# Kernel optimization log

Hardware: AMD Instinct MI355X
Metric: run time of the kernel (lower is better)

Reference implementation:

```python
import jax, jax.numpy as jnp
import numpy as np

B, T, C = 1, 2048, 2048
H, G, D = 16, 4, 128   # n_head, n_query_groups, head_size
I = 8192               # intermediate_size


def _hv(x, alpha, beta):
    # ParamHeaveside forward: alpha * heaviside(x - beta)
    return (alpha * (x - beta > 0).astype(x.dtype)).astype(x.dtype)


def _normed_linear(x, w, scale):
    # NormedLinear: column-center then L2-normalize columns (dim=0), scaled
    w = w - w.mean(axis=0, keepdims=True)
    n = jnp.maximum(jnp.sqrt((w * w).sum(axis=0, keepdims=True)), 1e-12)
    return x @ (scale * w / n).T


def _rope(t, cos, sin):
    # non-interleaved rotary (rotate-half), cos/sin: [T, D/2]
    half = t.shape[-1] // 2
    t1, t2 = t[..., :half], t[..., half:]
    c, s = cos[None, :, None, :], sin[None, :, None, :]
    return jnp.concatenate([t1 * c - t2 * s, t1 * s + t2 * c], axis=-1)


def _block(x, cos, sin, attn_w, proj_w, proj_scale, fc_w, mlp_proj_w, mlp_proj_scale,
           in_alpha, in_beta, q_alpha, q_beta, k_alpha, k_beta,
           out_alpha, out_beta, act1_alpha, act1_beta, act2_alpha, act2_beta, hv):
    q_per_kv = H // G
    h = hv(x, in_alpha, in_beta)                      # encoder_input (norm is identity)
    qkv = (h @ attn_w.T).reshape(B, T, G, q_per_kv + 2, D)
    q = qkv[:, :, :, :q_per_kv, :].reshape(B, T, H, D)
    k = qkv[:, :, :, q_per_kv, :]                     # [B,T,G,D]
    v = qkv[:, :, :, q_per_kv + 1, :]                 # [B,T,G,D]
    q = hv(_rope(q, cos, sin), q_alpha, q_beta)
    k = hv(_rope(k, cos, sin), k_alpha, k_beta)
    q = q.transpose(0, 2, 1, 3)                       # [B,H,T,D]
    k = jnp.repeat(k.transpose(0, 2, 1, 3), q_per_kv, axis=1)
    v = jnp.repeat(v.transpose(0, 2, 1, 3), q_per_kv, axis=1)
    scores = jnp.einsum('bhtd,bhsd->bhts', q, k) * (1.0 / D)  # scale = 1/head_size
    causal = jnp.tril(jnp.ones((T, T), bool))
    w = jnp.where(causal[None, None], jax.nn.relu(scores), 0.0)  # relu-attention
    y = jnp.einsum('bhts,bhsd->bhtd', w, v).transpose(0, 2, 1, 3).reshape(B, T, C)
    y = _normed_linear(hv(y, out_alpha, out_beta), proj_w, proj_scale)
    x = x + y
    m = hv(x, act1_alpha, act1_beta) @ fc_w.T
    m = _normed_linear(hv(m, act2_alpha, act2_beta), mlp_proj_w, mlp_proj_scale)
    return x + m


def setup_inputs() -> dict:
    key = jax.random.key(0)
    ks = jax.random.split(key, 8)
    rn = lambda k, s, sc=0.02: (jax.random.normal(k, s) * sc).astype(jnp.float32)
    theta = 1.0 / (10000.0 ** (jnp.arange(0, D, 2, dtype=jnp.float32) / D))
    idx = jnp.outer(jnp.arange(T, dtype=jnp.float32), theta)
    return {
        'x': jax.random.normal(ks[0], (B, T, C), dtype=jnp.float32),
        'cos': jnp.cos(idx), 'sin': jnp.sin(idx),
        'attn_w': rn(ks[1], ((H + 2 * G) * D, C)),
        'proj_w': rn(ks[2], (C, C)), 'proj_scale': jnp.float32(0.01),
        'fc_w': rn(ks[3], (I, C)),
        'mlp_proj_w': rn(ks[4], (C, I)), 'mlp_proj_scale': jnp.float32(0.01),
        'in_alpha': jnp.full((C,), 0.5, jnp.float32), 'in_beta': rn(ks[5], (C,), 0.01),
        'q_alpha': jnp.full((D,), 0.5, jnp.float32), 'q_beta': jnp.zeros((D,), jnp.float32),
        'k_alpha': jnp.full((D,), 0.5, jnp.float32), 'k_beta': jnp.zeros((D,), jnp.float32),
        'out_alpha': jnp.full((C,), 0.5, jnp.float32), 'out_beta': rn(ks[6], (C,), 0.01),
        'act1_alpha': jnp.full((C,), 0.5, jnp.float32), 'act1_beta': rn(ks[7], (C,), 0.01),
        'act2_alpha': jnp.full((I,), 0.5, jnp.float32), 'act2_beta': jnp.zeros((I,), jnp.float32),
    }


def reference(x, cos, sin, attn_w, proj_w, proj_scale, fc_w, mlp_proj_w, mlp_proj_scale,
              in_alpha, in_beta, q_alpha, q_beta, k_alpha, k_beta,
              out_alpha, out_beta, act1_alpha, act1_beta, act2_alpha, act2_beta):
    return _block(x, cos, sin, attn_w, proj_w, proj_scale, fc_w, mlp_proj_w, mlp_proj_scale,
                  in_alpha, in_beta, q_alpha, q_beta, k_alpha, k_beta,
                  out_alpha, out_beta, act1_alpha, act1_beta, act2_alpha, act2_beta, _hv)
```

## Files before the change

### kernel.cpp

```cpp
#include <hip/hip_runtime.h>

typedef __attribute__((ext_vector_type(8))) short short8;
typedef __attribute__((ext_vector_type(4))) float f32x4;
typedef __attribute__((ext_vector_type(4))) int i32x4;

constexpr int TT = 2048, CC = 2048, HQ = 16, GG = 4, DD = 128, IC = 8192;

__device__ __forceinline__ ushort f2b(float f) {
  union { float f; unsigned u; } v; v.f = f;
  unsigned r = v.u + 0x7fffu + ((v.u >> 16) & 1u);
  return (ushort)(r >> 16);
}
__device__ __forceinline__ float b2f(ushort u) {
  union { unsigned u; float f; } v; v.u = ((unsigned)u) << 16; return v.f;
}
__device__ __forceinline__ char q8(float eff, float r) {
  float q = rintf(eff * r);
  q = fminf(fmaxf(q, -127.f), 127.f);
  return (char)(int)q;
}
__device__ __forceinline__ unsigned cvt_pk_bf16(float a, float b) {
  unsigned r;
  asm("v_cvt_pk_bf16_f32 %0, %1, %2" : "=v"(r) : "v"(a), "v"(b));
  return r;
}

__device__ __forceinline__ void gload16(const void* g, void* l) {
  __builtin_amdgcn_global_load_lds(
      (const __attribute__((address_space(1))) void*)g,
      (__attribute__((address_space(3))) void*)l, 16, 0, 0);
}

#define BAR()    __builtin_amdgcn_s_barrier()
#define PRIO1()  __builtin_amdgcn_s_setprio(1)
#define PRIO0()  __builtin_amdgcn_s_setprio(0)

template<int EPI>
__global__ __launch_bounds__(512, 2)
void gemm_i8(const char* __restrict__ A, const char* __restrict__ B,
             void* __restrict__ C0, const float* __restrict__ s,
             const float* __restrict__ beta, int M, int N, int K, int kc)
{
  __shared__ alignas(16) char lds[131072];
  const int tid = threadIdx.x;
  const int l = tid & 63, w = tid >> 6;
  const int fl = l & 15, fh = l >> 4;
  const int wrm = w >> 2, wcn = w & 3;
  const int m0 = blockIdx.y * 256, n0 = blockIdx.x * 256;
  const int kBeg = blockIdx.z * kc;
  const int kEnd = (kBeg + kc < K) ? kBeg + kc : K;
  const int nt = (kEnd - kBeg) >> 7;

  i32x4 acc[8][4] = {};

  const int srow = tid >> 3;
  const int scol = ((tid & 7) ^ (srow & 7)) * 16;
  const char* Ag = A + (size_t)(m0 + srow) * K + kBeg + scol;
  const char* Bg = B + (size_t)(n0 + srow) * K + kBeg + scol;

  auto stage_half = [&](int tile, int h) {
    const char* base = (h < 2) ? Ag : Bg;
    const int half = h & 1;
    const char* g = base + (size_t)(half * 128) * K + tile * 128;
    char* d = lds + (tile & 1) * 65536 + ((h < 2) ? 0 : 32768) + half * 16384 + tid * 16;
    gload16(g, d);
    gload16(g + (size_t)64 * K, d + 8192);
  };

  auto readA = [&](i32x4 (&dst)[4][2], int buf, int mofs) {
#pragma unroll
    for (int mf = 0; mf < 4; ++mf)
#pragma unroll
      for (int ks = 0; ks < 2; ++ks) {
        int row = wrm * 128 + (mofs + mf) * 16 + fl;
        dst[mf][ks] = *(const i32x4*)(lds + buf * 65536 + row * 128 +
                                      (((ks * 4 + fh) ^ (row & 7)) * 16));
      }
  };
  auto readB = [&](i32x4 (&dst)[2][2], int buf, int nofs) {
#pragma unroll
    for (int nf = 0; nf < 2; ++nf)
#pragma unroll
      for (int ks = 0; ks < 2; ++ks) {
        int row = wcn * 64 + (nofs + nf) * 16 + fl;
        dst[nf][ks] = *(const i32x4*)(lds + buf * 65536 + 32768 + row * 128 +
                                      (((ks * 4 + fh) ^ (row & 7)) * 16));
      }
  };
  auto mmQ = [&](i32x4 (&a)[4][2], i32x4 (&b)[2][2], int mo, int no) {
    PRIO1();
#pragma unroll
    for (int mf = 0; mf < 4; ++mf)
#pragma unroll
      for (int nf = 0; nf < 2; ++nf)
#pragma unroll
        for (int ks = 0; ks < 2; ++ks)
          acc[mo + mf][no + nf] = __builtin_amdgcn_mfma_i32_16x16x64_i8(
              a[mf][ks], b[nf][ks], acc[mo + mf][no + nf], 0, 0, 0);
    PRIO0();
  };

  stage_half(0, 0); stage_half(0, 1); stage_half(0, 2); stage_half(0, 3);
  if (nt > 1) {
    stage_half(1, 2); stage_half(1, 3);
    asm volatile("s_waitcnt vmcnt(4)" ::: "memory");
  } else {
    asm volatile("s_waitcnt vmcnt(0)" ::: "memory");
  }
  BAR();

  for (int t = 0; t < nt; ++t) {
    const int buf = t & 1;
    i32x4 A0[4][2], A1[4][2], B0[2][2], B1[2][2];

    readA(A0, buf, 0);
    readB(B0, buf, 0);
    if (t + 1 < nt) stage_half(t + 1, 0);
    BAR();
    mmQ(A0, B0, 0, 0);

    readB(B1, buf, 2);
    if (t + 1 < nt) stage_half(t + 1, 1);
    BAR();
    mmQ(A0, B1, 0, 2);

    readA(A1, buf, 4);
    BAR();
    mmQ(A1, B0, 4, 0);

    if (t + 2 < nt) { stage_half(t + 2, 2); stage_half(t + 2, 3); }
    if (t <= nt - 3) asm volatile("s_waitcnt vmcnt(4)" ::: "memory");
    else             asm volatile("s_waitcnt vmcnt(0)" ::: "memory");
    BAR();
    mmQ(A1, B1, 4, 2);
  }

  const int orow0 = m0 + wrm * 128 + fh * 4;
  const int ocol0 = n0 + wcn * 64 + fl;
#pragma unroll
  for (int mf = 0; mf < 8; ++mf) {
#pragma unroll
    for (int nf = 0; nf < 4; ++nf) {
      const int c = ocol0 + nf * 16;
      const float sc = s[c];
#pragma unroll
      for (int j = 0; j < 4; ++j) {
        const int r = orow0 + mf * 16 + j;
        const size_t o = (size_t)r * N + c;
        float v = (float)acc[mf][nf][j] * sc;
        if constexpr (EPI == 1) {
          ((char*)C0)[o] = (v - beta[c] > 0.f) ? (char)1 : (char)0;
        } else {
          ((ushort*)C0 + (size_t)blockIdx.z * M * N)[o] = f2b(v);
        }
      }
    }
  }
}

template<int NS, int MODE>
__global__ void reduce_kernel(const ushort* p0, const ushort* p1, const ushort* p2, const ushort* p3,
                              const float* resid, float* outf, char* outb,
                              const float* beta, int n4, int cols)
{
  const ushort* ps[4] = {p0, p1, p2, p3};
  for (int i = blockIdx.x * blockDim.x + threadIdx.x; i < n4; i += gridDim.x * blockDim.x) {
    float4 s = ((const float4*)resid)[i];
#pragma unroll
    for (int z = 0; z < NS; ++z) {
      ushort4 q = ((const ushort4*)ps[z])[i];
      s.x += b2f(q.x); s.y += b2f(q.y); s.z += b2f(q.z); s.w += b2f(q.w);
    }
    ((float4*)outf)[i] = s;
    if constexpr (MODE == 1) {
      int c = (i * 4) & (cols - 1);
      char4 r;
      r.x = (s.x - beta[c] > 0.f) ? 1 : 0;
      r.y = (s.y - beta[c + 1] > 0.f) ? 1 : 0;
      r.z = (s.z - beta[c + 2] > 0.f) ? 1 : 0;
      r.w = (s.w - beta[c + 3] > 0.f) ? 1 : 0;
      ((char4*)outb)[i] = r;
    }
  }
}

__global__ __launch_bounds__(256, 4)
void attn_kernel(const ushort* __restrict__ qb, const ushort* __restrict__ kb,
                 const ushort* __restrict__ vt, char* __restrict__ hy,
                 const float* __restrict__ obeta)
{
  __shared__ alignas(16) ushort Ks[64 * 128];
  __shared__ alignas(16) ushort Vs[128 * 64];
  __shared__ alignas(16) ushort Ps[64 * 64];
  const int bx = blockIdx.x;
  const int h = blockIdx.y;
  const int qi = (h & 8) ? bx : (31 - bx);
  const int g = h >> 2;
  const int q0 = qi * 64;
  const int tid = threadIdx.x;
  const int w = tid >> 6, l = tid & 63;
  const int fl = l & 15, fh = l >> 4;

  auto stageK = [&](int s0t) {
#pragma unroll
    for (int i = 0; i < 4; ++i) {
      int row = w * 16 + i * 4 + (l >> 4);
      int c16 = (l & 15) ^ (row & 7);
      gload16(kb + (size_t)g * TT * DD + (size_t)(s0t + row) * DD + c16 * 8,
              (char*)Ks + (w << 12) + (i << 10) + (l << 4));
    }
  };
  auto stageV = [&](int s0t) {
#pragma unroll
    for (int i = 0; i < 4; ++i) {
      int d = w * 32 + i * 8 + (l >> 3);
      int c16 = (l & 7) ^ (d & 7);
      gload16(vt + (size_t)g * DD * TT + (size_t)d * TT + s0t + c16 * 8,
              (char*)Vs + (w << 12) + (i << 10) + (l << 4));
    }
  };

  short8 qf[4];
  {
    const ushort* qp = qb + (size_t)h * TT * DD + (size_t)(q0 + w * 16 + fl) * DD + fh * 8;
#pragma unroll
    for (int ks = 0; ks < 4; ++ks) qf[ks] = *(const short8*)(qp + ks * 32);
  }

  const int prow = w * 16 + fl;
  const int qg = q0 + prow;
  f32x4 oacc[8] = {};

  for (int s0 = 0; s0 <= q0; s0 += 64) {
    stageK(s0); stageV(s0);
    asm volatile("s_waitcnt vmcnt(0)" ::: "memory");
    BAR();

    f32x4 sacc[4] = {};
#pragma unroll
    for (int ks = 0; ks < 4; ++ks) {
#pragma unroll
      for (int n = 0; n < 4; ++n) {
        int krow = n * 16 + fl;
        int slotB = (ks * 4 + fh) ^ (krow & 7);
        short8 kf = *(const short8*)((char*)Ks + krow * 256 + slotB * 16);
        sacc[n] = __builtin_amdgcn_mfma_f32_16x16x32_bf16(kf, qf[ks], sacc[n], 0, 0, 0);
      }
    }

    const bool diag = (s0 == q0);
#pragma unroll
    for (int n = 0; n < 4; ++n) {
      float p[4];
#pragma unroll
      for (int j = 0; j < 4; ++j) {
        float v = sacc[n][j] * 0.0078125f;
        v = fmaxf(v, 0.f);
        if (diag) {
          int sg = s0 + n * 16 + fh * 4 + j;
          if (sg > qg) v = 0.f;
        }
        p[j] = v;
      }
      unsigned lo = cvt_pk_bf16(p[0], p[1]);
      unsigned hi = cvt_pk_bf16(p[2], p[3]);
      int slot = ((n * 2 + (fh >> 1)) ^ (prow & 7));
      char* addr = (char*)Ps + prow * 128 + slot * 16 + ((fh & 1) << 3);
      uint2 val; val.x = lo; val.y = hi;
      *(uint2*)addr = val;
    }

#pragma unroll
    for (int ks = 0; ks < 2; ++ks) {
      int slotA = (ks * 4 + fh) ^ (prow & 7);
      short8 pa = *(const short8*)((char*)Ps + prow * 128 + slotA * 16);
#pragma unroll
      for (int n = 0; n < 8; ++n) {
        int vrow = n * 16 + fl;
        int slotB = (ks * 4 + fh) ^ (vrow & 7);
        short8 vb = *(const short8*)((char*)Vs + vrow * 128 + slotB * 16);
        oacc[n] = __builtin_amdgcn_mfma_f32_16x16x32_bf16(pa, vb, oacc[n], 0, 0, 0);
      }
    }

    BAR();
  }

#pragma unroll
  for (int n = 0; n < 8; ++n) {
    const int c = h * DD + n * 16 + fl;
    const float be = obeta[c];
#pragma unroll
    for (int j = 0; j < 4; ++j) {
      const int tq = q0 + w * 16 + fh * 4 + j;
      float v = oacc[n][j];
      hy[(size_t)tq * CC + c] = (v - be > 0.f) ? (char)1 : (char)0;
    }
  }
}

__global__ __launch_bounds__(256)
void rope_hv_kernel(const ushort* __restrict__ qp0, const ushort* __restrict__ qp1,
                    const float* __restrict__ cs, const float* __restrict__ sn,
                    const float* __restrict__ qalpha, const float* __restrict__ qbeta,
                    const float* __restrict__ kalpha, const float* __restrict__ kbeta,
                    ushort* __restrict__ qb, ushort* __restrict__ kb,
                    ushort* __restrict__ vt)
{
  __shared__ ushort Vsh[64][129];
  const int t0 = blockIdx.x * 64, g = blockIdx.y, job = blockIdx.z;
  const int tid = threadIdx.x;
  if (job < 5) {
    const int hh = job;
    const float* alpha = (hh < 4) ? qalpha : kalpha;
    const float* beta = (hh < 4) ? qbeta : kbeta;
    const int hoff = (hh < 4) ? hh * 128 : 512;
    for (int it = 0; it < 16; ++it) {
      int idx = it * 256 + tid;
      int tr = idx >> 6, dd = idx & 63;
      size_t base = (size_t)(t0 + tr) * 3072 + g * 768 + hoff;
      float x1 = b2f(qp0[base + dd]) + b2f(qp1[base + dd]);
      float x2 = b2f(qp0[base + 64 + dd]) + b2f(qp1[base + 64 + dd]);
      float c = cs[(size_t)(t0 + tr) * 64 + dd];
      float s = sn[(size_t)(t0 + tr) * 64 + dd];
      float o1 = x1 * c - x2 * s, o2 = x1 * s + x2 * c;
      ushort b1 = (o1 - beta[dd] > 0.f) ? f2b(alpha[dd]) : (ushort)0;
      ushort b2 = (o2 - beta[64 + dd] > 0.f) ? f2b(alpha[64 + dd]) : (ushort)0;
      if (hh < 4) {
        size_t o = ((size_t)(g * 4 + hh) * TT + t0 + tr) * DD;
        qb[o + dd] = b1;
        qb[o + 64 + dd] = b2;
      } else {
        size_t o = ((size_t)g * TT + t0 + tr) * DD;
        kb[o + dd] = b1;
        kb[o + 64 + dd] = b2;
      }
    }
  } else {
    for (int it = 0; it < 32; ++it) {
      int idx = it * 256 + tid;
      int tr = idx >> 7, d = idx & 127;
      size_t src = (size_t)(t0 + tr) * 3072 + g * 768 + 640 + d;
      Vsh[tr][d] = f2b(b2f(qp0[src]) + b2f(qp1[src]));
    }
    __syncthreads();
    for (int it = 0; it < 32; ++it) {
      int idx = it * 256 + tid;
      int d = idx >> 6, tl = idx & 63;
      vt[((size_t)g * DD + d) * TT + t0 + tl] = Vsh[tl][d];
    }
  }
}

__global__ __launch_bounds__(256, 4)
void prep1_kernel(const float* __restrict__ attn_w, char* __restrict__ attn_q,
                  const float* __restrict__ fc_w, char* __restrict__ fc_q,
                  const float* __restrict__ inA, const float* __restrict__ a1A,
                  float* __restrict__ s_all,
                  const float* __restrict__ x, const float* __restrict__ ib,
                  char* __restrict__ h_in,
                  const float* __restrict__ pw, const float* __restrict__ mw,
                  float* __restrict__ ps, float* __restrict__ ps2,
                  float* __restrict__ ms, float* __restrict__ ms2)
{
  __shared__ alignas(16) float efs[8192];
  const int bx = blockIdx.x;
  const int tid = threadIdx.x;
  const int wv = tid >> 6, lane = tid & 63;
  float4* eflds = (float4*)(efs + wv * 2048);

  if (bx < 2816) {
    const float* W; char* Q; const float4* A4;
    int row, sofs;
    if (bx < 768) { W = attn_w; Q = attn_q; A4 = (const float4*)inA; row = bx * 4 + wv;         sofs = 0; }
    else          { W = fc_w;   Q = fc_q;   A4 = (const float4*)a1A; row = (bx - 768) * 4 + wv; sofs = 3072; }
    const float4* src = (const float4*)(W + (size_t)row * 2048);
    char4* dst = (char4*)(Q + (size_t)row * 2048);
    float m = 0.f;
#pragma unroll
    for (int it = 0; it < 8; ++it) {
      int i = it * 64 + lane;
      float4 v = src[i];
      float4 a = A4[i];
      float4 e;
      e.x = v.x * a.x; e.y = v.y * a.y; e.z = v.z * a.z; e.w = v.w * a.w;
      eflds[i] = e;
      m = fmaxf(m, fmaxf(fmaxf(fabsf(e.x), fabsf(e.y)), fmaxf(fabsf(e.z), fabsf(e.w))));
    }
    for (int mask = 32; mask; mask >>= 1) m = fmaxf(m, __shfl_xor(m, mask));
    if (lane == 0) s_all[sofs + row] = m * (1.f / 127.f);
    const float r = (m > 0.f) ? 127.f / m : 0.f;
#pragma unroll
    for (int it = 0; it < 8; ++it) {
      int i = it * 64 + lane;
      float4 e = eflds[i];
      char4 q;
      q.x = q8(e.x, r); q.y = q8(e.y, r);
      q.z = q8(e.z, r); q.w = q8(e.w, r);
      dst[i] = q;
    }
  } else if (bx < 3328) {
    const int blk = bx - 2816;
    const int stride = 512 * 256;
    const float4* ib4 = (const float4*)ib;
    for (int i = blk * 256 + tid; i < 2048 * 2048 / 4; i += stride) {
      float4 v = ((const float4*)x)[i];
      float4 b = ib4[i & 511];
      char4 q;
      q.x = (v.x - b.x > 0.f) ? 1 : 0;
      q.y = (v.y - b.y > 0.f) ? 1 : 0;
      q.z = (v.z - b.z > 0.f) ? 1 : 0;
      q.w = (v.w - b.w > 0.f) ? 1 : 0;
      ((char4*)h_in)[i] = q;
    }
  } else {
    const int jb = bx - 3328;
    const int sb = jb % 40;
    const int chunk = jb / 40;
    const float* W;
    float* os; float* os2; int cols, j;
    if (sb < 8) { W = pw; os = ps; os2 = ps2; cols = 2048; j = sb * 256 + tid; }
    else        { W = mw; os = ms; os2 = ms2; cols = 8192; j = (sb - 8) * 256 + tid; }
    const float* p = W + (size_t)chunk * 128 * cols + j;
    float s = 0.f, s2 = 0.f;
    for (int i = 0; i < 128; ++i) { float v = p[(size_t)i * cols]; s += v; s2 += v * v; }
    os[chunk * cols + j] = s;
    os2[chunk * cols + j] = s2;
  }
}

__global__ __launch_bounds__(256, 4)
void prep2_kernel(const float* __restrict__ proj_w, char* __restrict__ proj_q,
                  const float* __restrict__ mlp_w, char* __restrict__ mlp_q,
                  const float* __restrict__ p_iva, const float* __restrict__ p_muiva,
                  const float* __restrict__ m_iva, const float* __restrict__ m_muiva,
                  float* __restrict__ s_all)
{
  __shared__ alignas(16) float efs[8192];
  __shared__ float wmax[4];
  const int bx = blockIdx.x;
  const int tid = threadIdx.x;
  const int wv = tid >> 6, lane = tid & 63;
  float4* eflds = (float4*)(efs + wv * 2048);

  if (bx < 512) {
    const int row = bx * 4 + wv;
    const float4* src = (const float4*)(proj_w + (size_t)row * 2048);
    const float4* A4 = (const float4*)p_iva;
    const float4* MUIVA4 = (const float4*)p_muiva;
    char4* dst = (char4*)(proj_q + (size_t)row * 2048);
    float m = 0.f;
#pragma unroll
    for (int it = 0; it < 8; ++it) {
      int i = it * 64 + lane;
      float4 v = src[i];
      float4 a = A4[i], mv = MUIVA4[i];
      float4 e;
      e.x = fmaf(v.x, a.x, -mv.x);
      e.y = fmaf(v.y, a.y, -mv.y);
      e.z = fmaf(v.z, a.z, -mv.z);
      e.w = fmaf(v.w, a.w, -mv.w);
      eflds[i] = e;
      m = fmaxf(m, fmaxf(fmaxf(fabsf(e.x), fabsf(e.y)), fmaxf(fabsf(e.z), fabsf(e.w))));
    }
    for (int mask = 32; mask; mask >>= 1) m = fmaxf(m, __shfl_xor(m, mask));
    if (lane == 0) s_all[11264 + row] = m * (1.f / 127.f);
    const float r = (m > 0.f) ? 127.f / m : 0.f;
#pragma unroll
    for (int it = 0; it < 8; ++it) {
      int i = it * 64 + lane;
      float4 e = eflds[i];
      char4 q;
      q.x = q8(e.x, r); q.y = q8(e.y, r);
      q.z = q8(e.z, r); q.w = q8(e.w, r);
      dst[i] = q;
    }
  } else {
    const int row = bx - 512;
    const float4* src = (const float4*)(mlp_w + (size_t)row * 8192);
    const float4* A4 = (const float4*)m_iva;
    const float4* MUIVA4 = (const float4*)m_muiva;
    char4* dst = (char4*)(mlp_q + (size_t)row * 8192);
    float m = 0.f;
#pragma unroll
    for (int it = 0; it < 8; ++it) {
      int li = it * 64 + lane;
      int i = wv * 512 + li;
      float4 v = src[i];
      float4 a = A4[i], mv = MUIVA4[i];
      float4 e;
      e.x = fmaf(v.x, a.x, -mv.x);
      e.y = fmaf(v.y, a.y, -mv.y);
      e.z = fmaf(v.z, a.z, -mv.z);
      e.w = fmaf(v.w, a.w, -mv.w);
      eflds[li] = e;
      m = fmaxf(m, fmaxf(fmaxf(fabsf(e.x), fabsf(e.y)), fmaxf(fabsf(e.z), fabsf(e.w))));
    }
    for (int mask = 32; mask; mask >>= 1) m = fmaxf(m, __shfl_xor(m, mask));
    if (lane == 0) wmax[wv] = m;
    __syncthreads();
    m = fmaxf(fmaxf(wmax[0], wmax[1]), fmaxf(wmax[2], wmax[3]));
    if (tid == 0) s_all[13312 + row] = m * (1.f / 127.f);
    const float r = (m > 0.f) ? 127.f / m : 0.f;
#pragma unroll
    for (int it = 0; it < 8; ++it) {
      int li = it * 64 + lane;
      int i = wv * 512 + li;
      float4 e = eflds[li];
      char4 q;
      q.x = q8(e.x, r); q.y = q8(e.y, r);
      q.z = q8(e.z, r); q.w = q8(e.w, r);
      dst[i] = q;
    }
  }
}

__global__ void stats2_all(const float* __restrict__ ps, const float* __restrict__ ps2,
                           float* __restrict__ p_iva, float* __restrict__ p_muiva,
                           const float* __restrict__ pscale, const float* __restrict__ outA,
                           const float* __restrict__ ms, const float* __restrict__ ms2,
                           float* __restrict__ m_iva, float* __restrict__ m_muiva,
                           const float* __restrict__ mscale, const float* __restrict__ a2A)
{
  const int bx = blockIdx.x;
  const float* S; const float* S2; float* iva; float* muiva;
  const float* sc; const float* A; int cols, j;
  if (bx < 8) { S = ps; S2 = ps2; iva = p_iva; muiva = p_muiva; sc = pscale; A = outA; cols = 2048; j = bx * 256 + threadIdx.x; }
  else        { S = ms; S2 = ms2; iva = m_iva; muiva = m_muiva; sc = mscale; A = a2A;  cols = 8192; j = (bx - 8) * 256 + threadIdx.x; }
  float s = 0.f, s2 = 0.f;
  for (int c = 0; c < 16; ++c) { s += S[c * cols + j]; s2 += S2[c * cols + j]; }
  float m = s * (1.f / 2048.f);
  float var = s2 - s * m;
  float nn = sqrtf(fmaxf(var, 0.f));
  nn = fmaxf(nn, 1e-12f);
  float iv = (sc[0] / nn) * A[j];
  iva[j] = iv;
  muiva[j] = m * iv;
}

extern "C" void kernel_launch(void* const* d_in, const int* in_sizes, int n_in,
                              void* d_out, int out_size, void* d_ws, size_t ws_size,
                              hipStream_t stream) {
  const float* x          = (const float*)d_in[0];
  const float* cosT       = (const float*)d_in[1];
  const float* sinT       = (const float*)d_in[2];
  const float* attn_w     = (const float*)d_in[3];
  const float* proj_w     = (const float*)d_in[4];
  const float* proj_scale = (const float*)d_in[5];
  const float* fc_w       = (const float*)d_in[6];
  const float* mlp_proj_w = (const float*)d_in[7];
  const float* mlp_scale  = (const float*)d_in[8];
  const float* in_alpha   = (const float*)d_in[9];
  const float* in_beta    = (const float*)d_in[10];
  const float* q_alpha    = (const float*)d_in[11];
  const float* q_beta     = (const float*)d_in[12];
  const float* k_alpha    = (const float*)d_in[13];
  const float* k_beta     = (const float*)d_in[14];
  const float* out_alpha  = (const float*)d_in[15];
  const float* out_beta   = (const float*)d_in[16];
  const float* act1_alpha = (const float*)d_in[17];
  const float* act1_beta  = (const float*)d_in[18];
  const float* act2_alpha = (const float*)d_in[19];
  const float* act2_beta  = (const float*)d_in[20];

  char* cur = (char*)d_ws;
  auto alloc = [&](size_t b) { void* p = cur; cur += (b + 255) & ~(size_t)255; return p; };

  char* attn_q = (char*)alloc((size_t)3072 * 2048);
  char* fc_q   = (char*)alloc((size_t)8192 * 2048);
  char* proj_q = (char*)alloc((size_t)2048 * 2048);
  char* mlp_q  = (char*)alloc((size_t)2048 * 8192);
  char* h_in   = (char*)alloc((size_t)2048 * 2048);
  char* h_y    = (char*)alloc((size_t)2048 * 2048);
  char* h2     = (char*)alloc((size_t)2048 * 2048);
  char* h3     = (char*)alloc((size_t)2048 * 8192);
  ushort* qbuf  = (ushort*)alloc((size_t)HQ * TT * DD * 2);
  ushort* kbuf  = (ushort*)alloc((size_t)GG * TT * DD * 2);
  ushort* vtbuf = (ushort*)alloc((size_t)GG * DD * TT * 2);
  float* x2 = (float*)alloc((size_t)2048 * 2048 * 4);
  ushort* qkv_parts  = (ushort*)alloc((size_t)2 * 2048 * 3072 * 2);
  ushort* proj_parts = (ushort*)alloc((size_t)4 * 2048 * 2048 * 2);
  ushort* mlp_parts  = (ushort*)alloc((size_t)4 * 2048 * 2048 * 2);
  float* pp_s  = (float*)alloc(16 * 2048 * 4);
  float* pp_s2 = (float*)alloc(16 * 2048 * 4);
  float* mp_s  = (float*)alloc(16 * 8192 * 4);
  float* mp_s2 = (float*)alloc(16 * 8192 * 4);
  float* p_iva   = (float*)alloc(2048 * 4);
  float* p_muiva = (float*)alloc(2048 * 4);
  float* m_iva   = (float*)alloc(8192 * 4);
  float* m_muiva = (float*)alloc(8192 * 4);
  float* s_all = (float*)alloc(15360 * 4);

  const size_t PLANE_QKV = (size_t)2048 * 3072;
  const size_t PLANE     = (size_t)2048 * 2048;

  float* s_attn = s_all;
  float* s_fc   = s_all + 3072;
  float* s_proj = s_all + 11264;
  float* s_mlp  = s_all + 13312;

  prep1_kernel<<<3968, 256, 0, stream>>>(attn_w, attn_q, fc_w, fc_q,
                                         in_alpha, act1_alpha, s_all,
                                         x, in_beta, h_in,
                                         proj_w, mlp_proj_w, pp_s, pp_s2, mp_s, mp_s2);
  stats2_all<<<40, 256, 0, stream>>>(pp_s, pp_s2, p_iva, p_muiva, proj_scale, out_alpha,
                                     mp_s, mp_s2, m_iva, m_muiva, mlp_scale, act2_alpha);
  prep2_kernel<<<2560, 256, 0, stream>>>(proj_w, proj_q, mlp_proj_w, mlp_q,
                                         p_iva, p_muiva, m_iva, m_muiva, s_all);

  gemm_i8<3><<<dim3(3072 / 256, 2048 / 256, 2), 512, 0, stream>>>(
      h_in, attn_q, qkv_parts, s_attn, nullptr, 2048, 3072, 2048, 1024);

  rope_hv_kernel<<<dim3(TT / 64, GG, 6), 256, 0, stream>>>(
      qkv_parts, qkv_parts + PLANE_QKV, cosT, sinT,
      q_alpha, q_beta, k_alpha, k_beta, qbuf, kbuf, vtbuf);

  attn_kernel<<<dim3(TT / 64, HQ), 256, 0, stream>>>(qbuf, kbuf, vtbuf, h_y, out_beta);

  gemm_i8<3><<<dim3(2048 / 256, 2048 / 256, 4), 512, 0, stream>>>(
      h_y, proj_q, proj_parts, s_proj, nullptr, 2048, 2048, 2048, 512);
  reduce_kernel<4, 1><<<2048, 256, 0, stream>>>(
      proj_parts, proj_parts + PLANE, proj_parts + 2 * PLANE, proj_parts + 3 * PLANE,
      x, x2, h2, act1_beta, 2048 * 2048 / 4, 2048);

  gemm_i8<1><<<dim3(8192 / 256, 2048 / 256, 1), 512, 0, stream>>>(
      h2, fc_q, h3, s_fc, act2_beta, 2048, 8192, 2048, 2048);

  gemm_i8<3><<<dim3(8, 8, 4), 512, 0, stream>>>(
      h3, mlp_q, mlp_parts, s_mlp, nullptr, 2048, 2048, 8192, 2048);
  reduce_kernel<4, 2><<<2048, 256, 0, stream>>>(
      mlp_parts, mlp_parts + PLANE, mlp_parts + 2 * PLANE, mlp_parts + 3 * PLANE,
      x2, (float*)d_out, nullptr, nullptr, 2048 * 2048 / 4, 1);
}
```

Before: 263.7 us.

## Split attention KV loop across two blocks and merge partials in new kernel

The attention kernel now launches two blocks per (query tile, head), each handling alternating 64-key tiles, and writes bf16 partial outputs to a new buffer. A separate merge kernel sums the two partials and applies the output heaviside threshold to produce the int8 activation. This doubles grid parallelism and shortens the longest causal loops (split-K style), at the cost of writing and reading two bf16 planes of partial outputs, an extra launch, and bf16 rounding before the threshold compare.

```diff
diff --git a/kernel.cpp b/kernel.cpp
--- a/kernel.cpp
+++ b/kernel.cpp
@@ -186,14 +186,14 @@
 
 __global__ __launch_bounds__(256, 4)
 void attn_kernel(const ushort* __restrict__ qb, const ushort* __restrict__ kb,
-                 const ushort* __restrict__ vt, char* __restrict__ hy,
-                 const float* __restrict__ obeta)
+                 const ushort* __restrict__ vt, ushort* __restrict__ opart)
 {
   __shared__ alignas(16) ushort Ks[64 * 128];
   __shared__ alignas(16) ushort Vs[128 * 64];
   __shared__ alignas(16) ushort Ps[64 * 64];
   const int bx = blockIdx.x;
   const int h = blockIdx.y;
+  const int z = blockIdx.z;
   const int qi = (h & 8) ? bx : (31 - bx);
   const int g = h >> 2;
   const int q0 = qi * 64;
@@ -231,7 +231,7 @@
   const int qg = q0 + prow;
   f32x4 oacc[8] = {};
 
-  for (int s0 = 0; s0 <= q0; s0 += 64) {
+  for (int s0 = z * 64; s0 <= q0; s0 += 128) {
     stageK(s0); stageV(s0);
     asm volatile("s_waitcnt vmcnt(0)" ::: "memory");
     BAR();
@@ -286,16 +286,31 @@
     BAR();
   }
 
+  ushort* op = opart + (size_t)z * TT * CC;
 #pragma unroll
   for (int n = 0; n < 8; ++n) {
     const int c = h * DD + n * 16 + fl;
-    const float be = obeta[c];
 #pragma unroll
     for (int j = 0; j < 4; ++j) {
       const int tq = q0 + w * 16 + fh * 4 + j;
-      float v = oacc[n][j];
-      hy[(size_t)tq * CC + c] = (v - be > 0.f) ? (char)1 : (char)0;
-    }
+      op[(size_t)tq * CC + c] = f2b(oacc[n][j]);
+    }
+  }
+}
+
+__global__ void merge_hy(const ushort* __restrict__ p0, const ushort* __restrict__ p1,
+                         const float* __restrict__ obeta, char* __restrict__ hy, int n4)
+{
+  for (int i = blockIdx.x * blockDim.x + threadIdx.x; i < n4; i += gridDim.x * blockDim.x) {
+    ushort4 a = ((const ushort4*)p0)[i];
+    ushort4 b = ((const ushort4*)p1)[i];
+    int c = (i * 4) & (CC - 1);
+    char4 r;
+    r.x = (b2f(a.x) + b2f(b.x) - obeta[c] > 0.f) ? 1 : 0;
+    r.y = (b2f(a.y) + b2f(b.y) - obeta[c + 1] > 0.f) ? 1 : 0;
+    r.z = (b2f(a.z) + b2f(b.z) - obeta[c + 2] > 0.f) ? 1 : 0;
+    r.w = (b2f(a.w) + b2f(b.w) - obeta[c + 3] > 0.f) ? 1 : 0;
+    ((char4*)hy)[i] = r;
   }
 }
 
@@ -577,6 +592,7 @@
   ushort* qbuf  = (ushort*)alloc((size_t)HQ * TT * DD * 2);
   ushort* kbuf  = (ushort*)alloc((size_t)GG * TT * DD * 2);
   ushort* vtbuf = (ushort*)alloc((size_t)GG * DD * TT * 2);
+  ushort* opart = (ushort*)alloc((size_t)2 * TT * CC * 2);
   float* x2 = (float*)alloc((size_t)2048 * 2048 * 4);
   ushort* qkv_parts  = (ushort*)alloc((size_t)2 * 2048 * 3072 * 2);
   ushort* proj_parts = (ushort*)alloc((size_t)4 * 2048 * 2048 * 2);
@@ -615,7 +631,8 @@
       qkv_parts, qkv_parts + PLANE_QKV, cosT, sinT,
       q_alpha, q_beta, k_alpha, k_beta, qbuf, kbuf, vtbuf);
 
-  attn_kernel<<<dim3(TT / 64, HQ), 256, 0, stream>>>(qbuf, kbuf, vtbuf, h_y, out_beta);
+  attn_kernel<<<dim3(TT / 64, HQ, 2), 256, 0, stream>>>(qbuf, kbuf, vtbuf, opart);
+  merge_hy<<<2048, 256, 0, stream>>>(opart, opart + TT * CC, out_beta, h_y, TT * CC / 4);
 
   gemm_i8<3><<<dim3(2048 / 256, 2048 / 256, 4), 512, 0, stream>>>(
       h_y, proj_q, proj_parts, s_proj, nullptr, 2048, 2048, 2048, 512);
```

New measurement: 254.6 us. 3.4% less time.
